# Kernel optimization log

Measured on AMD Instinct MI355X. Metric: run time of the kernel, lower is better.

Reference implementation:

```python
import jax, jax.numpy as jnp
import numpy as np

RPN_BBOX_STD_DEV = np.array([0.1, 0.1, 0.2, 0.2], dtype=np.float32)
PRE_NMS_LIMIT = 6000
PROPOSAL_COUNT = 1000
NMS_THRESHOLD = 0.7
BATCH = 8
NUM_ANCHORS = 261888


def setup_inputs() -> dict:
    key = jax.random.key(0)
    k1, k2, k3, k4 = jax.random.split(key, 4)
    fg = jax.random.uniform(k1, (BATCH, NUM_ANCHORS), dtype=jnp.float32)
    rpn_probs = jnp.stack([1.0 - fg, fg], axis=-1)  # [B, N, 2] (bg, fg)
    rpn_bbox = jax.random.normal(k2, (BATCH, NUM_ANCHORS, 4), dtype=jnp.float32) * 0.5
    # valid normalized anchors: y_min < y_max, x_min < x_max, inside [0, 1]
    mins = jax.random.uniform(k3, (BATCH, NUM_ANCHORS, 2), minval=0.0, maxval=0.85)
    size = jax.random.uniform(k4, (BATCH, NUM_ANCHORS, 2), minval=0.02, maxval=0.15)
    anchors = jnp.concatenate([mins, mins + size], axis=-1)  # [B, N, 4]
    return {"rpn_probs": rpn_probs, "rpn_bbox": rpn_bbox, "anchors": anchors}


def apply_box_deltas(boxes, deltas):
    # boxes: [..., (y1, x1, y2, x2)], deltas: [..., (dy, dx, log(dh), log(dw))]
    h = boxes[..., 2] - boxes[..., 0]
    w = boxes[..., 3] - boxes[..., 1]
    cy = boxes[..., 0] + 0.5 * h + deltas[..., 0] * h
    cx = boxes[..., 1] + 0.5 * w + deltas[..., 1] * w
    h = h * jnp.exp(deltas[..., 2])
    w = w * jnp.exp(deltas[..., 3])
    y1 = cy - 0.5 * h
    x1 = cx - 0.5 * w
    return jnp.stack([y1, x1, y1 + h, x1 + w], axis=-1)


def pairwise_iou(boxes):
    # boxes: [N, 4] -> iou [N, N]
    y1, x1, y2, x2 = boxes[:, 0], boxes[:, 1], boxes[:, 2], boxes[:, 3]
    area = (y2 - y1) * (x2 - x1)
    ih = jnp.maximum(jnp.minimum(y2[:, None], y2[None, :]) - jnp.maximum(y1[:, None], y1[None, :]), 0.0)
    iw = jnp.maximum(jnp.minimum(x2[:, None], x2[None, :]) - jnp.maximum(x1[:, None], x1[None, :]), 0.0)
    inter = ih * iw
    union = area[:, None] + area[None, :] - inter
    return jnp.where(union > 0.0, inter / union, 0.0)


def nms_single(boxes):
    # boxes: [K, 4], already sorted by score descending (top_k sorted=True).
    # Greedy NMS: a box is suppressed if it overlaps (IoU > thresh) a kept,
    # higher-scoring box. Sequential suppression via lax.scan over rows.
    K = boxes.shape[0]
    iou = pairwise_iou(boxes)  # [K, K]
    order = jnp.arange(K)

    def step(keep, i):
        suppress = keep[i] & (iou[i] > NMS_THRESHOLD) & (order > i)
        return keep & ~suppress, None

    keep, _ = jax.lax.scan(step, jnp.ones((K,), dtype=bool), order)
    # gather kept boxes in score order, pad with zeros to PROPOSAL_COUNT
    rank = jnp.cumsum(keep) - 1
    valid = keep & (rank < PROPOSAL_COUNT)
    dest = jnp.where(valid, rank, PROPOSAL_COUNT)  # invalid rows -> scratch row
    out = jnp.zeros((PROPOSAL_COUNT + 1, 4), boxes.dtype).at[dest].set(boxes)
    return out[:PROPOSAL_COUNT]


def reference(rpn_probs, rpn_bbox, anchors):
    scores = rpn_probs[:, :, 1]  # fg prob [B, N]
    deltas = rpn_bbox * jnp.asarray(RPN_BBOX_STD_DEV).reshape(1, 1, 4)
    k = min(PRE_NMS_LIMIT, anchors.shape[1])
    top_scores, idx = jax.lax.top_k(scores, k)  # sorted descending, [B, K]
    deltas_k = jnp.take_along_axis(deltas, idx[..., None], axis=1)   # [B, K, 4]
    anchors_k = jnp.take_along_axis(anchors, idx[..., None], axis=1)  # [B, K, 4]
    boxes = jnp.clip(apply_box_deltas(anchors_k, deltas_k), 0.0, 1.0)
    proposals = jax.vmap(nms_single)(boxes)  # [B, PROPOSAL_COUNT, 4]
    return proposals
```

## Files before the change

### kernel.cpp

```cpp
#include <hip/hip_runtime.h>
#include <hip/hip_bf16.h>

typedef unsigned long long ull;

constexpr int BATCH = 8;
constexpr int NA    = 261888;
constexpr int KSEL  = 6000;
constexpr int PROP  = 1000;
constexpr int CAP   = 8192;
constexpr int NBINS = 8192;
constexpr int HB    = 16;
constexpr int NB    = (KSEL + 63) / 64;
constexpr int NWP   = 94;
constexpr int NBLK  = 94;
constexpr int NBLK2 = 47;

constexpr size_t OFF_CNT   = 0;
constexpr size_t OFF_TSEL  = 512;
constexpr size_t OFF_BOXES = 544;
constexpr size_t OFF_MASK  = 769024;
constexpr size_t OFF_DIAG  = OFF_MASK + 36096000;
constexpr size_t OFF_SUP   = OFF_DIAG + 385024;
constexpr size_t OFF_KEYS  = OFF_MASK;
constexpr size_t OFF_HIST  = OFF_MASK + 2097152;

__device__ __forceinline__ int score_bin(float s) {
  int b = (int)(s * (float)NBINS);
  if (b < 0) b = 0;
  if (b > NBINS - 1) b = NBINS - 1;
  return b;
}

__global__ __launch_bounds__(256) void hist_kernel(const float4* __restrict__ probs4,
                                                   unsigned int* __restrict__ hist,
                                                   int* __restrict__ cnt,
                                                   ull* __restrict__ keys) {
  __shared__ unsigned int lh[NBINS];
  for (int i = threadIdx.x; i < NBINS; i += 256) lh[i] = 0u;
  int fb = blockIdx.y * HB + blockIdx.x;
  if (threadIdx.x == 0) cnt[fb] = 0;
  {
    ull* kp = keys + (size_t)fb * 512;
    for (int i = threadIdx.x; i < 512; i += 256) kp[i] = ~0ull;
  }
  __syncthreads();
  int b = blockIdx.y;
  const float4* p = probs4 + (size_t)b * (NA / 2);
  for (int a = blockIdx.x * 256 + threadIdx.x; a < NA / 2; a += HB * 256) {
    float4 v = p[a];
    atomicAdd(&lh[score_bin(v.y)], 1u);
    atomicAdd(&lh[score_bin(v.w)], 1u);
  }
  __syncthreads();
  unsigned int* gh = hist + ((size_t)b * HB + blockIdx.x) * NBINS;
  for (int i = threadIdx.x; i < NBINS; i += 256) gh[i] = lh[i];
}

__global__ __launch_bounds__(256) void thresh_kernel(const unsigned int* __restrict__ hist,
                                                     int* __restrict__ tsel) {
  constexpr int GR = NBINS / 256;
  __shared__ unsigned int ch[NBINS];
  __shared__ unsigned int gsum[256];
  int b = blockIdx.x;
  const unsigned int* h = hist + (size_t)b * HB * NBINS;
  for (int bin = threadIdx.x; bin < NBINS; bin += 256) {
    unsigned int s = 0;
    for (int k = 0; k < HB; ++k) s += h[(size_t)k * NBINS + bin];
    ch[bin] = s;
  }
  __syncthreads();
  unsigned int s = 0;
  int g0 = threadIdx.x * GR;
  for (int i = 0; i < GR; ++i) s += ch[g0 + i];
  gsum[threadIdx.x] = s;
  __syncthreads();
  if (threadIdx.x == 0) {
    unsigned int acc = 0;
    int g = 255;
    for (; g > 0; --g) {
      if (acc + gsum[g] >= (unsigned)KSEL) break;
      acc += gsum[g];
    }
    int t = g * GR;
    for (int bin = g * GR + GR - 1; bin >= g * GR; --bin) {
      acc += ch[bin];
      if (acc >= (unsigned)KSEL) { t = bin; break; }
    }
    tsel[b] = t;
  }
}

__global__ __launch_bounds__(256) void compact_kernel(const float4* __restrict__ probs4,
                                                      const int* __restrict__ tsel,
                                                      int* __restrict__ cnt,
                                                      ull* __restrict__ keys) {
  __shared__ int lcnt, lbase;
  __shared__ ull lbuf[2048];
  int b = blockIdx.y;
  int t = tsel[b];
  if (threadIdx.x == 0) lcnt = 0;
  __syncthreads();
  const float4* p = probs4 + (size_t)b * (NA / 2);
  for (int a = blockIdx.x * blockDim.x + threadIdx.x; a < NA / 2; a += gridDim.x * blockDim.x) {
    float4 v = p[a];
    if (score_bin(v.y) >= t) {
      int pos = atomicAdd(&lcnt, 1);
      unsigned int ib = ~__float_as_uint(v.y);
      lbuf[pos] = ((ull)ib << 32) | (unsigned int)(2 * a);
    }
    if (score_bin(v.w) >= t) {
      int pos = atomicAdd(&lcnt, 1);
      unsigned int ib = ~__float_as_uint(v.w);
      lbuf[pos] = ((ull)ib << 32) | (unsigned int)(2 * a + 1);
    }
  }
  __syncthreads();
  if (threadIdx.x == 0) lbase = atomicAdd(&cnt[b * 16], lcnt);
  __syncthreads();
  int n = lcnt, base = lbase;
  ull* kb = keys + (size_t)b * CAP;
  for (int i = threadIdx.x; i < n; i += 256) {
    int pos = base + i;
    if (pos < CAP) kb[pos] = lbuf[i];
  }
}

__global__ __launch_bounds__(256) void rankscatter_kernel(const float4* __restrict__ anchors4,
                                                          const float4* __restrict__ bbox4,
                                                          const int* __restrict__ cnt,
                                                          const ull* __restrict__ keys,
                                                          float4* __restrict__ boxes4) {
#pragma clang fp contract(off)
  __shared__ ull tile[1024];
  int b = blockIdx.y;
  int n = cnt[b * 16];
  if (n > CAP) n = CAP;
  int i = blockIdx.x * 256 + threadIdx.x;
  const ull* kb = keys + (size_t)b * CAP;
  ull my = (i < CAP) ? kb[(i < n) ? i : 0] : ~0ull;
  if (i >= n) my = ~0ull;
  unsigned int r = 0;
  int ntile = (n + 1023) & ~1023;
  for (int j0 = 0; j0 < ntile; j0 += 1024) {
    for (int k = threadIdx.x; k < 1024; k += 256) tile[k] = kb[j0 + k];
    __syncthreads();
#pragma unroll 16
    for (int k = 0; k < 1024; ++k) r += (tile[k] < my) ? 1u : 0u;
    __syncthreads();
  }
  if (i >= n || r >= (unsigned)KSEL) return;
  int a = (int)(unsigned int)(my & 0xffffffffull);
  float4 anc = anchors4[(size_t)b * NA + a];
  float4 d   = bbox4[(size_t)b * NA + a];
  float h = anc.z - anc.x;
  float w = anc.w - anc.y;
  float dy = d.x * 0.1f, dx = d.y * 0.1f, dh = d.z * 0.2f, dw = d.w * 0.2f;
  float cy = (anc.x + (0.5f * h)) + (dy * h);
  float cx = (anc.y + (0.5f * w)) + (dx * w);
  float h2 = h * expf(dh);
  float w2 = w * expf(dw);
  float y1 = cy - 0.5f * h2;
  float x1 = cx - 0.5f * w2;
  float y2 = y1 + h2;
  float x2 = x1 + w2;
  y1 = fminf(fmaxf(y1, 0.f), 1.f);
  x1 = fminf(fmaxf(x1, 0.f), 1.f);
  y2 = fminf(fmaxf(y2, 0.f), 1.f);
  x2 = fminf(fmaxf(x2, 0.f), 1.f);
  boxes4[(size_t)b * KSEL + r] = make_float4(y1, x1, y2, x2);
}

__global__ __launch_bounds__(256) void mask_kernel(const float4* __restrict__ boxes4,
                                                   ull* __restrict__ mask,
                                                   ull* __restrict__ diagT,
                                                   ull* __restrict__ superT) {
#pragma clang fp contract(off)
  int cx = blockIdx.x, rb2 = blockIdx.y, b = blockIdx.z;
  int w0 = 2 * rb2;
  int cb0 = w0 + 4 * cx;
  if (cb0 >= NWP) return;
  __shared__ float4 colbox[4][64];
  __shared__ float  colca[4][64];
  __shared__ ull wtile[128][5];
  int tid = threadIdx.x, wv = tid >> 6, l = tid & 63;
  int cb = cb0 + wv;
  int rA = rb2 * 128 + l, rB = rA + 64;
  float4 zero = make_float4(0.f, 0.f, 0.f, 0.f);
  float4 boxA = (rA < KSEL) ? boxes4[(size_t)b * KSEL + rA] : zero;
  float4 boxB = (rB < KSEL) ? boxes4[(size_t)b * KSEL + rB] : zero;
  float areaA = (boxA.z - boxA.x) * (boxA.w - boxA.y);
  float areaB = (boxB.z - boxB.x) * (boxB.w - boxB.y);
  int c = cb * 64 + l;
  float4 cload = (cb < NB && c < KSEL) ? boxes4[(size_t)b * KSEL + c] : zero;
  colbox[wv][l] = cload;
  colca[wv][l] = (cload.z - cload.x) * (cload.w - cload.y);
  __syncthreads();
  ull bitsA = 0ull, bitsB = 0ull;
  if (cb < NB) {
#pragma unroll
    for (int u = 0; u < 64; ++u) {
      float4 cbx = colbox[wv][u];
      float ca = colca[wv][u];
      {
        float ih = fmaxf(fminf(boxA.z, cbx.z) - fmaxf(boxA.x, cbx.x), 0.f);
        float iw = fmaxf(fminf(boxA.w, cbx.w) - fmaxf(boxA.y, cbx.y), 0.f);
        float inter = ih * iw;
        float uni = (areaA + ca) - inter;
        float d = fmaf(-0.7f, uni, inter);
        float tt = 6e-7f * uni;
        bool keep;
        if (__builtin_fabsf(d) <= tt) keep = (inter / uni) > 0.7f;
        else keep = d > 0.f;
        if (keep) bitsA |= (1ull << u);
      }
      {
        float ih = fmaxf(fminf(boxB.z, cbx.z) - fmaxf(boxB.x, cbx.x), 0.f);
        float iw = fmaxf(fminf(boxB.w, cbx.w) - fmaxf(boxB.y, cbx.y), 0.f);
        float inter = ih * iw;
        float uni = (areaB + ca) - inter;
        float d = fmaf(-0.7f, uni, inter);
        float tt = 6e-7f * uni;
        bool keep;
        if (__builtin_fabsf(d) <= tt) keep = (inter / uni) > 0.7f;
        else keep = d > 0.f;
        if (keep) bitsB |= (1ull << u);
      }
    }
    if (cb == w0) {
      bitsA &= (l == 63) ? 0ull : (~0ull << (l + 1));
      ull colT = 0ull;
#pragma unroll
      for (int k = 0; k < 64; ++k) {
        ull bk = __ballot(((bitsA >> k) & 1ull) != 0ull);
        if (l == k) colT = bk;
      }
      diagT[((size_t)b * NBLK + w0) * 64 + l] = colT;
    }
    if (cb == w0 + 1) {
      superT[((size_t)b * NBLK + w0) * 64 + l] = bitsA;
      bitsB &= (l == 63) ? 0ull : (~0ull << (l + 1));
      ull colT = 0ull;
#pragma unroll
      for (int k = 0; k < 64; ++k) {
        ull bk = __ballot(((bitsB >> k) & 1ull) != 0ull);
        if (l == k) colT = bk;
      }
      diagT[((size_t)b * NBLK + w0 + 1) * 64 + l] = colT;
    }
    if (cb == w0 + 2) {
      superT[((size_t)b * NBLK + w0 + 1) * 64 + l] = bitsB;
    }
  }
  wtile[l][wv] = bitsA;
  wtile[l + 64][wv] = bitsB;
  __syncthreads();
  int base_row = rb2 * 128;
#pragma unroll
  for (int pass = 0; pass < 2; ++pass) {
    int idx = pass * 256 + tid;
    int rr = idx >> 2, w = idx & 3;
    int row = base_row + rr;
    if (row < KSEL && cb0 + w < NWP)
      mask[((size_t)b * KSEL + row) * NWP + cb0 + w] = wtile[rr][w];
  }
}

__global__ __launch_bounds__(1024, 1) void scan_kernel(const float4* __restrict__ boxes4,
                                                       const ull* __restrict__ mask,
                                                       const ull* __restrict__ diagT,
                                                       const ull* __restrict__ superT,
                                                       float4* __restrict__ out4) {
  __shared__ ull ldiagT[NBLK * 64];
  __shared__ ull lsuper[NBLK * 64];
  __shared__ ull S[96];
  __shared__ ull S_urg;
  __shared__ int klist[2][64];
  __shared__ int skeep[1024];
  __shared__ int s_kept, s_done, s_klen[2];
  int b = blockIdx.x;
  int tid = threadIdx.x;
  int lane = tid & 63;
  const ull* mb = mask + (size_t)b * KSEL * NWP;

  const ull* dt = diagT + (size_t)b * NBLK * 64;
  const ull* st = superT + (size_t)b * NBLK * 64;
  for (int i = tid; i < NBLK * 64; i += 1024) { ldiagT[i] = dt[i]; lsuper[i] = st[i]; }
  if (tid < 96) S[tid] = 0ull;
  if (tid == 0) { s_kept = 0; s_done = 0; s_klen[0] = 0; s_klen[1] = 0; S_urg = 0ull; }
  __syncthreads();

  for (int n = 0; n < NBLK; ++n) {
    if (tid < 64) {
      ull Sn = S[n] | S_urg;
      int i0 = n * 64;
      ull colT = ldiagT[i0 + lane];
      ull sd = (n + 1 < NBLK) ? lsuper[i0 + lane] : 0ull;
      int nval = KSEL - i0;
      ull valid = (nval >= 64) ? ~0ull : ((1ull << nval) - 1ull);
      ull A = ~Sn & valid;
      ull K = 0ull;
      int kept = s_kept;
      int done = 0;
      while (A) {
        int u = __builtin_ctzll(A);
        ++kept;
        K |= (1ull << u);
        if (kept >= PROP) { done = 1; break; }
        ull sup = __ballot(((colT >> u) & 1ull) != 0ull);
        A &= ~(sup | (1ull << u));
      }
      int klen = __builtin_popcountll(K);
      int kbase = kept - klen;
      if ((K >> lane) & 1ull) {
        int rank = __builtin_popcountll(K & ((1ull << lane) - 1ull));
        skeep[kbase + rank] = i0 + lane;
        klist[n & 1][rank] = i0 + lane;
      }
      int klp = (klen + 7) & ~7;
      if (klen > 0 && lane >= klen && lane < klp)
        klist[n & 1][lane] = i0 + __builtin_ctzll(K);
      unsigned ulo = (unsigned)sd, uhi = (unsigned)(sd >> 32);
      if (!((K >> lane) & 1ull)) { ulo = 0u; uhi = 0u; }
#pragma unroll
      for (int m = 1; m < 64; m <<= 1) {
        ulo |= (unsigned)__shfl_xor((int)ulo, m, 64);
        uhi |= (unsigned)__shfl_xor((int)uhi, m, 64);
      }
      if (lane == 0) {
        s_klen[n & 1] = klen;
        S_urg = (ull)ulo | ((ull)uhi << 32);
        s_kept = kept;
        if (done || n == NBLK - 1) s_done = 1;
      }
    } else {
      int prev = (n & 1) ^ 1;
      int kl = s_klen[prev];
      int lt = tid - 64;
      int wi = lt >> 3;
      int sub = lt & 7;
      int w = n + 1 + wi;
      if (kl > 0 && w < NB) {
        const int* kp = klist[prev];
        int klp8 = (kl + 7) & ~7;
        int per = klp8 >> 3;
        int base = sub * per;
        ull acc = 0ull;
#pragma unroll 8
        for (int ri = 0; ri < per; ++ri)
          acc |= mb[(size_t)kp[base + ri] * NWP + w];
        if (acc) atomicOr(&S[w], acc);
      }
    }
    __syncthreads();
    if (s_done) break;
  }

  int fin = s_kept;
  if (fin > PROP) fin = PROP;
  const float4* bx = boxes4 + (size_t)b * KSEL;
  for (int r2 = tid; r2 < PROP; r2 += 1024) {
    float4 v = make_float4(0.f, 0.f, 0.f, 0.f);
    if (r2 < fin) v = bx[skeep[r2]];
    out4[(size_t)b * PROP + r2] = v;
  }
}

extern "C" void kernel_launch(void* const* d_in, const int* in_sizes, int n_in,
                              void* d_out, int out_size, void* d_ws, size_t ws_size,
                              hipStream_t stream) {
  const float4* probs4  = (const float4*)d_in[0];
  const float4* bbox4   = (const float4*)d_in[1];
  const float4* anchors4= (const float4*)d_in[2];
  float4* out4 = (float4*)d_out;
  char* ws = (char*)d_ws;

  int* cnt           = (int*)(ws + OFF_CNT);
  int* tsel          = (int*)(ws + OFF_TSEL);
  float4* boxes4     = (float4*)(ws + OFF_BOXES);
  ull* maskw         = (ull*)(ws + OFF_MASK);
  ull* diagT         = (ull*)(ws + OFF_DIAG);
  ull* superT        = (ull*)(ws + OFF_SUP);
  ull* keys          = (ull*)(ws + OFF_KEYS);
  unsigned int* hist = (unsigned int*)(ws + OFF_HIST);

  hipLaunchKernelGGL(hist_kernel,        dim3(HB, BATCH),      dim3(256),  0, stream, probs4, hist, cnt, keys);
  hipLaunchKernelGGL(thresh_kernel,      dim3(BATCH),          dim3(256),  0, stream, hist, tsel);
  hipLaunchKernelGGL(compact_kernel,     dim3(128, BATCH),     dim3(256),  0, stream, probs4, tsel, cnt, keys);
  hipLaunchKernelGGL(rankscatter_kernel, dim3(32, BATCH),      dim3(256),  0, stream, anchors4, bbox4, cnt, keys, boxes4);
  hipLaunchKernelGGL(mask_kernel,        dim3(24, NBLK2, BATCH), dim3(256), 0, stream, boxes4, maskw, diagT, superT);
  hipLaunchKernelGGL(scan_kernel,        dim3(BATCH),          dim3(1024), 0, stream, boxes4, maskw, diagT, superT, out4);
}
```

Measured before the change: 325.1 us.

## Split NMS into two phases, computing the off-diagonal mask only for kept rows

The IoU bitmask no longer covers the full upper triangle. Mask words for rows in the first half against columns in the second half are dropped. The scan now runs in two phases. After phase 0 a new maskx kernel computes suppression of the second-half columns using only the boxes already kept, and ORs the result into a global suppression vector. This roughly halves mask storage and mask compute and writes, in exchange for two extra launches and a sequential dependency between them.

```diff
diff --git a/kernel.cpp b/kernel.cpp
--- a/kernel.cpp
+++ b/kernel.cpp
@@ -10,17 +10,24 @@
 constexpr int CAP   = 8192;
 constexpr int NBINS = 8192;
 constexpr int HB    = 16;
-constexpr int NB    = (KSEL + 63) / 64;
-constexpr int NWP   = 94;
 constexpr int NBLK  = 94;
-constexpr int NBLK2 = 47;
+constexpr int NBLK0 = 48;
+constexpr int SPLIT = 3072;
+constexpr int MC0_W = 48;
+constexpr int MC1_W = 46;
+constexpr int MC0_SZ = SPLIT * MC0_W;
+constexpr int MC1_SZ = (KSEL - SPLIT) * MC1_W;
+constexpr int MBATCH = MC0_SZ + MC1_SZ;
 
 constexpr size_t OFF_CNT   = 0;
 constexpr size_t OFF_TSEL  = 512;
-constexpr size_t OFF_BOXES = 544;
-constexpr size_t OFF_MASK  = 769024;
-constexpr size_t OFF_DIAG  = OFF_MASK + 36096000;
+constexpr size_t OFF_KC    = 544;
+constexpr size_t OFF_BOXES = 608;
+constexpr size_t OFF_MASK  = 768608;
+constexpr size_t OFF_DIAG  = OFF_MASK + 18057216;
 constexpr size_t OFF_SUP   = OFF_DIAG + 385024;
+constexpr size_t OFF_SKG   = OFF_SUP + 385024;
+constexpr size_t OFF_GS    = OFF_SKG + 32768;
 constexpr size_t OFF_KEYS  = OFF_MASK;
 constexpr size_t OFF_HIST  = OFF_MASK + 2097152;
 
@@ -34,7 +41,8 @@
 __global__ __launch_bounds__(256) void hist_kernel(const float4* __restrict__ probs4,
                                                    unsigned int* __restrict__ hist,
                                                    int* __restrict__ cnt,
-                                                   ull* __restrict__ keys) {
+                                                   ull* __restrict__ keys,
+                                                   ull* __restrict__ gS) {
   __shared__ unsigned int lh[NBINS];
   for (int i = threadIdx.x; i < NBINS; i += 256) lh[i] = 0u;
   int fb = blockIdx.y * HB + blockIdx.x;
@@ -42,6 +50,9 @@
   {
     ull* kp = keys + (size_t)fb * 512;
     for (int i = threadIdx.x; i < 512; i += 256) kp[i] = ~0ull;
+  }
+  if (fb == 0) {
+    for (int i = threadIdx.x; i < BATCH * NBLK; i += 256) gS[i] = 0ull;
   }
   __syncthreads();
   int b = blockIdx.y;
@@ -171,14 +182,17 @@
 }
 
 __global__ __launch_bounds__(256) void mask_kernel(const float4* __restrict__ boxes4,
-                                                   ull* __restrict__ mask,
+                                                   ull* __restrict__ maskw,
                                                    ull* __restrict__ diagT,
-                                                   ull* __restrict__ superT) {
+                                                   ull* __restrict__ superT,
+                                                   int rb2Base, int rowBase, int wordBase,
+                                                   int wordLim, int stride, int chunkOff) {
 #pragma clang fp contract(off)
-  int cx = blockIdx.x, rb2 = blockIdx.y, b = blockIdx.z;
+  int cx = blockIdx.x, b = blockIdx.z;
+  int rb2 = rb2Base + blockIdx.y;
   int w0 = 2 * rb2;
   int cb0 = w0 + 4 * cx;
-  if (cb0 >= NWP) return;
+  if (cb0 >= wordLim) return;
   __shared__ float4 colbox[4][64];
   __shared__ float  colca[4][64];
   __shared__ ull wtile[128][5];
@@ -191,12 +205,12 @@
   float areaA = (boxA.z - boxA.x) * (boxA.w - boxA.y);
   float areaB = (boxB.z - boxB.x) * (boxB.w - boxB.y);
   int c = cb * 64 + l;
-  float4 cload = (cb < NB && c < KSEL) ? boxes4[(size_t)b * KSEL + c] : zero;
+  float4 cload = (cb < wordLim && c < KSEL) ? boxes4[(size_t)b * KSEL + c] : zero;
   colbox[wv][l] = cload;
   colca[wv][l] = (cload.z - cload.x) * (cload.w - cload.y);
   __syncthreads();
   ull bitsA = 0ull, bitsB = 0ull;
-  if (cb < NB) {
+  if (cb < wordLim) {
 #pragma unroll
     for (int u = 0; u < 64; ++u) {
       float4 cbx = colbox[wv][u];
@@ -260,15 +274,74 @@
     int idx = pass * 256 + tid;
     int rr = idx >> 2, w = idx & 3;
     int row = base_row + rr;
-    if (row < KSEL && cb0 + w < NWP)
-      mask[((size_t)b * KSEL + row) * NWP + cb0 + w] = wtile[rr][w];
-  }
-}
-
+    int cw = cb0 + w;
+    if (row < KSEL && cw < wordLim)
+      maskw[(size_t)b * MBATCH + chunkOff + (size_t)(row - rowBase) * stride + (cw - wordBase)]
+        = wtile[rr][w];
+  }
+}
+
+__global__ __launch_bounds__(64) void maskx_kernel(const float4* __restrict__ boxes4,
+                                                   const int* __restrict__ skeepG,
+                                                   const int* __restrict__ kc,
+                                                   ull* __restrict__ gS) {
+#pragma clang fp contract(off)
+  __shared__ float4 colbox[64];
+  __shared__ float  colca[64];
+  int b = blockIdx.z;
+  int kept0 = kc[b * 2];
+  int rg = blockIdx.y;
+  if (rg * 64 >= kept0) return;
+  int l = threadIdx.x;
+  int w = NBLK0 + blockIdx.x;
+  int c = w * 64 + l;
+  float4 zero = make_float4(0.f, 0.f, 0.f, 0.f);
+  float4 cld = (c < KSEL) ? boxes4[(size_t)b * KSEL + c] : zero;
+  colbox[l] = cld;
+  colca[l] = (cld.z - cld.x) * (cld.w - cld.y);
+  __syncthreads();
+  int idx = rg * 64 + l;
+  ull bits = 0ull;
+  if (idx < kept0) {
+    int r = skeepG[b * 1024 + idx];
+    float4 rb = boxes4[(size_t)b * KSEL + r];
+    float rA = (rb.z - rb.x) * (rb.w - rb.y);
+#pragma unroll
+    for (int u = 0; u < 64; ++u) {
+      float4 cbx = colbox[u];
+      float ca = colca[u];
+      float ih = fmaxf(fminf(rb.z, cbx.z) - fmaxf(rb.x, cbx.x), 0.f);
+      float iw = fmaxf(fminf(rb.w, cbx.w) - fmaxf(rb.y, cbx.y), 0.f);
+      float inter = ih * iw;
+      float uni = (rA + ca) - inter;
+      float d = fmaf(-0.7f, uni, inter);
+      float tt = 6e-7f * uni;
+      bool keep;
+      if (__builtin_fabsf(d) <= tt) keep = (inter / uni) > 0.7f;
+      else keep = d > 0.f;
+      if (keep) bits |= (1ull << u);
+    }
+  }
+  unsigned lo = (unsigned)bits, hi = (unsigned)(bits >> 32);
+#pragma unroll
+  for (int m = 1; m < 64; m <<= 1) {
+    lo |= (unsigned)__shfl_xor((int)lo, m, 64);
+    hi |= (unsigned)__shfl_xor((int)hi, m, 64);
+  }
+  if (l == 0) {
+    ull v = (ull)lo | ((ull)hi << 32);
+    if (v) atomicOr(&gS[b * NBLK + w], v);
+  }
+}
+
+template<int PHASE>
 __global__ __launch_bounds__(1024, 1) void scan_kernel(const float4* __restrict__ boxes4,
-                                                       const ull* __restrict__ mask,
+                                                       const ull* __restrict__ maskw,
                                                        const ull* __restrict__ diagT,
                                                        const ull* __restrict__ superT,
+                                                       int* __restrict__ skeepG,
+                                                       int* __restrict__ kc,
+                                                       const ull* __restrict__ gS,
                                                        float4* __restrict__ out4) {
   __shared__ ull ldiagT[NBLK * 64];
   __shared__ ull lsuper[NBLK * 64];
@@ -280,16 +353,26 @@
   int b = blockIdx.x;
   int tid = threadIdx.x;
   int lane = tid & 63;
-  const ull* mb = mask + (size_t)b * KSEL * NWP;
+  const ull* mb = maskw + (size_t)b * MBATCH;
+  const int nB = PHASE ? NBLK0 : 0;
+  const int nE = PHASE ? NBLK : NBLK0;
 
   const ull* dt = diagT + (size_t)b * NBLK * 64;
   const ull* st = superT + (size_t)b * NBLK * 64;
-  for (int i = tid; i < NBLK * 64; i += 1024) { ldiagT[i] = dt[i]; lsuper[i] = st[i]; }
-  if (tid < 96) S[tid] = 0ull;
-  if (tid == 0) { s_kept = 0; s_done = 0; s_klen[0] = 0; s_klen[1] = 0; S_urg = 0ull; }
-  __syncthreads();
-
-  for (int n = 0; n < NBLK; ++n) {
+  for (int i = nB * 64 + tid; i < nE * 64; i += 1024) { ldiagT[i] = dt[i]; lsuper[i] = st[i]; }
+  if (PHASE == 0) {
+    if (tid < 96) S[tid] = 0ull;
+    if (tid == 0) { s_kept = 0; s_done = 0; s_klen[0] = 0; s_klen[1] = 0; S_urg = 0ull; }
+  } else {
+    int k0 = kc[b * 2], d0 = kc[b * 2 + 1];
+    if (tid < 96) S[tid] = (tid >= NBLK0 && tid < NBLK) ? gS[b * NBLK + tid] : 0ull;
+    for (int i = tid; i < k0; i += 1024) skeep[i] = skeepG[b * 1024 + i];
+    if (tid == 0) { s_kept = k0; s_done = d0; s_klen[0] = 0; s_klen[1] = 0; S_urg = 0ull; }
+  }
+  __syncthreads();
+
+  for (int n = nB; n < nE; ++n) {
+    if (s_done) break;
     if (tid < 64) {
       ull Sn = S[n] | S_urg;
       int i0 = n * 64;
@@ -330,7 +413,7 @@
         s_klen[n & 1] = klen;
         S_urg = (ull)ulo | ((ull)uhi << 32);
         s_kept = kept;
-        if (done || n == NBLK - 1) s_done = 1;
+        if (done) s_done = 1;
       }
     } else {
       int prev = (n & 1) ^ 1;
@@ -339,29 +422,39 @@
       int wi = lt >> 3;
       int sub = lt & 7;
       int w = n + 1 + wi;
-      if (kl > 0 && w < NB) {
+      if (kl > 0 && w < nE) {
         const int* kp = klist[prev];
         int klp8 = (kl + 7) & ~7;
         int per = klp8 >> 3;
         int base = sub * per;
         ull acc = 0ull;
 #pragma unroll 8
-        for (int ri = 0; ri < per; ++ri)
-          acc |= mb[(size_t)kp[base + ri] * NWP + w];
+        for (int ri = 0; ri < per; ++ri) {
+          int r = kp[base + ri];
+          size_t addr = (PHASE == 0) ? ((size_t)r * MC0_W + w)
+                                     : ((size_t)MC0_SZ + (size_t)(r - SPLIT) * MC1_W + (w - NBLK0));
+          acc |= mb[addr];
+        }
         if (acc) atomicOr(&S[w], acc);
       }
     }
     __syncthreads();
-    if (s_done) break;
-  }
-
-  int fin = s_kept;
-  if (fin > PROP) fin = PROP;
-  const float4* bx = boxes4 + (size_t)b * KSEL;
-  for (int r2 = tid; r2 < PROP; r2 += 1024) {
-    float4 v = make_float4(0.f, 0.f, 0.f, 0.f);
-    if (r2 < fin) v = bx[skeep[r2]];
-    out4[(size_t)b * PROP + r2] = v;
+  }
+
+  if (PHASE == 0) {
+    int k0 = s_kept;
+    if (k0 > PROP) k0 = PROP;
+    for (int i = tid; i < k0; i += 1024) skeepG[b * 1024 + i] = skeep[i];
+    if (tid == 0) { kc[b * 2] = k0; kc[b * 2 + 1] = s_done; }
+  } else {
+    int fin = s_kept;
+    if (fin > PROP) fin = PROP;
+    const float4* bx = boxes4 + (size_t)b * KSEL;
+    for (int r2 = tid; r2 < PROP; r2 += 1024) {
+      float4 v = make_float4(0.f, 0.f, 0.f, 0.f);
+      if (r2 < fin) v = bx[skeep[r2]];
+      out4[(size_t)b * PROP + r2] = v;
+    }
   }
 }
 
@@ -376,17 +469,28 @@
 
   int* cnt           = (int*)(ws + OFF_CNT);
   int* tsel          = (int*)(ws + OFF_TSEL);
+  int* kc            = (int*)(ws + OFF_KC);
   float4* boxes4     = (float4*)(ws + OFF_BOXES);
   ull* maskw         = (ull*)(ws + OFF_MASK);
   ull* diagT         = (ull*)(ws + OFF_DIAG);
   ull* superT        = (ull*)(ws + OFF_SUP);
+  int* skeepG        = (int*)(ws + OFF_SKG);
+  ull* gS            = (ull*)(ws + OFF_GS);
   ull* keys          = (ull*)(ws + OFF_KEYS);
   unsigned int* hist = (unsigned int*)(ws + OFF_HIST);
 
-  hipLaunchKernelGGL(hist_kernel,        dim3(HB, BATCH),      dim3(256),  0, stream, probs4, hist, cnt, keys);
-  hipLaunchKernelGGL(thresh_kernel,      dim3(BATCH),          dim3(256),  0, stream, hist, tsel);
-  hipLaunchKernelGGL(compact_kernel,     dim3(128, BATCH),     dim3(256),  0, stream, probs4, tsel, cnt, keys);
-  hipLaunchKernelGGL(rankscatter_kernel, dim3(32, BATCH),      dim3(256),  0, stream, anchors4, bbox4, cnt, keys, boxes4);
-  hipLaunchKernelGGL(mask_kernel,        dim3(24, NBLK2, BATCH), dim3(256), 0, stream, boxes4, maskw, diagT, superT);
-  hipLaunchKernelGGL(scan_kernel,        dim3(BATCH),          dim3(1024), 0, stream, boxes4, maskw, diagT, superT, out4);
-}
+  hipLaunchKernelGGL(hist_kernel,        dim3(HB, BATCH),    dim3(256), 0, stream, probs4, hist, cnt, keys, gS);
+  hipLaunchKernelGGL(thresh_kernel,      dim3(BATCH),        dim3(256), 0, stream, hist, tsel);
+  hipLaunchKernelGGL(compact_kernel,     dim3(128, BATCH),   dim3(256), 0, stream, probs4, tsel, cnt, keys);
+  hipLaunchKernelGGL(rankscatter_kernel, dim3(32, BATCH),    dim3(256), 0, stream, anchors4, bbox4, cnt, keys, boxes4);
+  hipLaunchKernelGGL(mask_kernel, dim3(12, 24, BATCH), dim3(256), 0, stream,
+                     boxes4, maskw, diagT, superT, 0, 0, 0, NBLK0, MC0_W, 0);
+  hipLaunchKernelGGL(mask_kernel, dim3(12, 23, BATCH), dim3(256), 0, stream,
+                     boxes4, maskw, diagT, superT, 24, SPLIT, NBLK0, NBLK, MC1_W, MC0_SZ);
+  scan_kernel<0><<<dim3(BATCH), dim3(1024), 0, stream>>>(boxes4, maskw, diagT, superT,
+                                                         skeepG, kc, gS, out4);
+  hipLaunchKernelGGL(maskx_kernel, dim3(NBLK - NBLK0, 16, BATCH), dim3(64), 0, stream,
+                     boxes4, skeepG, kc, gS);
+  scan_kernel<1><<<dim3(BATCH), dim3(1024), 0, stream>>>(boxes4, maskw, diagT, superT,
+                                                         skeepG, kc, gS, out4);
+}
```

Measured after the change: 313.1 us. -3.7%, faster.
